# Kernel tuning notes

Measured on AMD Instinct MI355X. Metric: run time of the kernel, lower is better.

## Reference

```python
import jax, jax.numpy as jnp
import numpy as np

NUM_HEADS = 8
EPS_NORM = 1e-12
EPS_DEN = 1e-5


def _l2norm(x):
    # torch F.normalize(dim=-1): x / max(||x||_2, eps)
    n = jnp.sqrt(jnp.sum(x * x, axis=-1, keepdims=True))
    return x / jnp.maximum(n, EPS_NORM)


def _fast_attention(qs, ks, vs):
    # qs, ks, vs: (B', L, H, m) where L is the attended axis length
    qs = _l2norm(qs)
    ks = _l2norm(ks)
    L = qs.shape[1]
    # KV outer-product summed over the attended axis: (B', H, m, d)
    kvs = jnp.einsum('blhm,blhd->bhmd', ks, vs)
    num = jnp.einsum('bnhm,bhmd->bnhd', qs, kvs) + L * vs
    ks_sum = jnp.sum(ks, axis=1)                       # (B', H, m)
    den = jnp.einsum('bnhm,bhm->bnh', qs, ks_sum)[..., None] + L
    den = jnp.maximum(den, EPS_DEN)                    # clamp_min
    return num / den                                   # (B', L, H, m)


def setup_inputs() -> dict:
    key = jax.random.key(0)
    k1, k2, k3, k4 = jax.random.split(key, 4)
    B, T, N, D = 4, 24, 2048, 256
    x = jax.random.normal(k1, (B, T, N, D), dtype=jnp.float32)
    w_qkv = jax.random.normal(k2, (3 * D, D), dtype=jnp.float32) / np.sqrt(D)
    w_out = jax.random.normal(k3, (D, 2 * D), dtype=jnp.float32) / np.sqrt(2 * D)
    b_out = jax.random.normal(k4, (D,), dtype=jnp.float32) * 0.01
    return {"x": x, "w_qkv": w_qkv, "w_out": w_out, "b_out": b_out}


def reference(x, w_qkv, w_out, b_out):
    B, T, N, D = x.shape
    H = NUM_HEADS
    hd = D // H
    qkv = jnp.einsum('btnd,ed->btne', x, w_qkv)        # (B,T,N,3D), no bias
    q, k, v = jnp.split(qkv, 3, axis=-1)
    # heads: split last dim into (H, hd) chunks == reshape
    qh = q.reshape(B, T, N, H, hd)
    kh = k.reshape(B, T, N, H, hd)
    vh = v.reshape(B, T, N, H, hd)

    # spatial attention: attend over N, batch over (B*T)
    out_s = _fast_attention(qh.reshape(B * T, N, H, hd),
                            kh.reshape(B * T, N, H, hd),
                            vh.reshape(B * T, N, H, hd))
    out_s = out_s.reshape(B, T, N, D)

    # temporal attention: attend over T, batch over (B*N)
    qt = jnp.transpose(qh, (0, 2, 1, 3, 4)).reshape(B * N, T, H, hd)
    kt = jnp.transpose(kh, (0, 2, 1, 3, 4)).reshape(B * N, T, H, hd)
    vt = jnp.transpose(vh, (0, 2, 1, 3, 4)).reshape(B * N, T, H, hd)
    out_t = _fast_attention(qt, kt, vt).reshape(B, N, T, D)
    out_t = jnp.transpose(out_t, (0, 2, 1, 3))         # (B,T,N,D)

    out = jnp.concatenate([out_s, out_t], axis=-1)     # (B,T,N,2D)
    return jnp.einsum('btnf,df->btnd', out, w_out) + b_out
```

## Files before the change

### kernel.cpp

```cpp
#include <hip/hip_runtime.h>
#include <hip/hip_bf16.h>
#include <cstdint>
#include <cstddef>

#define B_   4
#define T_   24
#define NN_  2048
#define D_   256
#define H_   8
#define HD_  32
#define BT_  (B_*T_)
#define MTOK (B_*T_*NN_)

using bf16 = __hip_bfloat16;

typedef __attribute__((ext_vector_type(8))) short bf16x8;
typedef __attribute__((ext_vector_type(4))) float f32x4;

__device__ __forceinline__ float bf2f(bf16 v) { return __bfloat162float(v); }
__device__ __forceinline__ ushort f2bfu(float x) {
  bf16 t = __float2bfloat16(x);
  return *(ushort*)&t;
}
__device__ __forceinline__ float bfu2f(ushort u) {
  return __uint_as_float((uint32_t)u << 16);
}
__device__ __forceinline__ float rsq_fast(float ss) {
  return __builtin_amdgcn_rsqf(fmaxf(ss, 1e-24f));
}
__device__ __forceinline__ float rcp_fast(float x) {
  return __builtin_amdgcn_rcpf(x);
}

__device__ __forceinline__ void async_copy16(const void* g, void* l) {
  __builtin_amdgcn_global_load_lds(
      (const __attribute__((address_space(1))) void*)g,
      (__attribute__((address_space(3))) void*)l,
      16, 0, 0);
}

#define UNPK8(u, F0,F1,F2,F3,F4,F5,F6,F7)                       \
  const float F0 = __uint_as_float((u).x << 16);                \
  const float F1 = __uint_as_float((u).x & 0xffff0000u);        \
  const float F2 = __uint_as_float((u).y << 16);                \
  const float F3 = __uint_as_float((u).y & 0xffff0000u);        \
  const float F4 = __uint_as_float((u).z << 16);                \
  const float F5 = __uint_as_float((u).z & 0xffff0000u);        \
  const float F6 = __uint_as_float((u).w << 16);                \
  const float F7 = __uint_as_float((u).w & 0xffff0000u);

__global__ void k_convert(const float* __restrict__ in, bf16* __restrict__ out, int n4) {
  int i = blockIdx.x * blockDim.x + threadIdx.x;
  if (i < n4) {
    float4 v = ((const float4*)in)[i];
    bf16 t[4] = {__float2bfloat16(v.x), __float2bfloat16(v.y),
                 __float2bfloat16(v.z), __float2bfloat16(v.w)};
    ((ushort4*)out)[i] = *(ushort4*)t;
  }
}

template<int KD, bool OUTF32>
__global__ __launch_bounds__(256, 2)
void k_gemm(const bf16* __restrict__ A, const bf16* __restrict__ Bw,
            void* __restrict__ Cout, const float* __restrict__ bias, int ncols) {
  __shared__ bf16 As[128 * 64];
  __shared__ bf16 Bs[128 * 64];
  const int tid  = threadIdx.x;
  const int wave = tid >> 6, lane = tid & 63;
  const int quad = lane >> 4, l16 = lane & 15;
  const long row0 = (long)blockIdx.x * 128;
  const long col0 = (long)blockIdx.y * 128;
  const int wm = (wave & 1) * 64, wn = (wave >> 1) * 64;
  const int srow = lane >> 3;
  const int skb  = (lane & 7) * 8;

  f32x4 acc[4][4];
  const f32x4 z = {0.f, 0.f, 0.f, 0.f};
#pragma unroll
  for (int a = 0; a < 4; ++a)
#pragma unroll
    for (int b = 0; b < 4; ++b) acc[a][b] = z;

  for (int k0 = 0; k0 < KD; k0 += 64) {
#pragma unroll
    for (int i = 0; i < 4; ++i) {
      const int c = wave * 4 + i;
      const int r = c * 8 + srow;
      async_copy16(A  + (row0 + r) * KD + k0 + skb, (char*)As + c * 1024);
      async_copy16(Bw + (col0 + r) * KD + k0 + skb, (char*)Bs + c * 1024);
    }
    __syncthreads();
#pragma unroll
    for (int kk = 0; kk < 64; kk += 32) {
      bf16x8 af[4], bfr[4];
#pragma unroll
      for (int i = 0; i < 4; ++i)
        af[i] = *(const bf16x8*)(As + (wm + i * 16 + l16) * 64 + kk + quad * 8);
#pragma unroll
      for (int i = 0; i < 4; ++i)
        bfr[i] = *(const bf16x8*)(Bs + (wn + i * 16 + l16) * 64 + kk + quad * 8);
#pragma unroll
      for (int mi = 0; mi < 4; ++mi)
#pragma unroll
        for (int ni = 0; ni < 4; ++ni)
          acc[mi][ni] = __builtin_amdgcn_mfma_f32_16x16x32_bf16(af[mi], bfr[ni], acc[mi][ni], 0, 0, 0);
    }
    __syncthreads();
  }

#pragma unroll
  for (int mi = 0; mi < 4; ++mi)
#pragma unroll
    for (int ni = 0; ni < 4; ++ni) {
      const long colg = col0 + wn + ni * 16 + l16;
#pragma unroll
      for (int r = 0; r < 4; ++r) {
        const long rowg = row0 + wm + mi * 16 + quad * 4 + r;
        const float v = acc[mi][ni][r];
        if (OUTF32) {
          ((float*)Cout)[rowg * ncols + colg] = v + bias[colg];
        } else {
          ((bf16*)Cout)[rowg * ncols + colg] = __float2bfloat16(v);
        }
      }
    }
}

__global__ __launch_bounds__(256)
void k_spatial_stats(bf16* __restrict__ qkv, float* __restrict__ stats) {
  const int bt = blockIdx.x, h = blockIdx.y;
  const int tid = threadIdx.x;
  const int wave = tid >> 6, lane = tid & 63;
  __shared__ float lk[256][36];
  __shared__ float lv[256][36];
  const int mg = lane >> 3, dg = lane & 7;
  const int m0 = mg * 4, d0 = dg * 4;
  float acc[4][4] = {};
  float ssum[4] = {0.f, 0.f, 0.f, 0.f};

  for (int c = wave * 64; c < NN_; c += 256) {
    const size_t row = ((size_t)bt * NN_ + c + lane) * 768;
    bf16 kb[32], vb[32];
    const uint4* kp = (const uint4*)(qkv + row + 256 + h * 32);
    const uint4* vp = (const uint4*)(qkv + row + 512 + h * 32);
#pragma unroll
    for (int j = 0; j < 4; ++j) { ((uint4*)kb)[j] = kp[j]; ((uint4*)vb)[j] = vp[j]; }
    float kf[32]; float ss = 0.f;
#pragma unroll
    for (int j = 0; j < 32; ++j) { kf[j] = bf2f(kb[j]); ss += kf[j] * kf[j]; }
    const float sc = rsq_fast(ss);
#pragma unroll
    for (int j = 0; j < 32; ++j) kf[j] *= sc;
    ushort kh16[32];
#pragma unroll
    for (int j = 0; j < 32; ++j) kh16[j] = f2bfu(kf[j]);
    uint4* dstk = (uint4*)(qkv + row + 256 + h * 32);
#pragma unroll
    for (int j = 0; j < 4; ++j) dstk[j] = ((uint4*)kh16)[j];

    float vf[32];
#pragma unroll
    for (int j = 0; j < 32; ++j) vf[j] = bf2f(vb[j]);
    const int lrow = wave * 64 + lane;
#pragma unroll
    for (int j = 0; j < 8; ++j) {
      ((float4*)lk[lrow])[j] = ((float4*)kf)[j];
      ((float4*)lv[lrow])[j] = ((float4*)vf)[j];
    }
    __syncthreads();
#pragma unroll 2
    for (int t = 0; t < 64; ++t) {
      const int tr = wave * 64 + t;
      const float4 ka = *(const float4*)&lk[tr][m0];
      const float4 va = *(const float4*)&lv[tr][d0];
      const float km[4] = {ka.x, ka.y, ka.z, ka.w};
      const float vm[4] = {va.x, va.y, va.z, va.w};
#pragma unroll
      for (int i = 0; i < 4; ++i) {
        ssum[i] += km[i];
#pragma unroll
        for (int j = 0; j < 4; ++j) acc[i][j] += km[i] * vm[j];
      }
    }
    __syncthreads();
  }

  float* rbuf = (float*)lk;
  float* wb = rbuf + wave * 1056;
#pragma unroll
  for (int i = 0; i < 4; ++i) {
    float4 o = {acc[i][0], acc[i][1], acc[i][2], acc[i][3]};
    *(float4*)&wb[(m0 + i) * 32 + d0] = o;
  }
  if (dg == 0) {
#pragma unroll
    for (int i = 0; i < 4; ++i) wb[1024 + m0 + i] = ssum[i];
  }
  __syncthreads();
  float* base = stats + ((size_t)bt * H_ + h) * 1056;
  for (int e = tid; e < 1056; e += 256)
    base[e] = rbuf[e] + rbuf[1056 + e] + rbuf[2112 + e] + rbuf[3168 + e];
}

#define SP_CHUNK 64
__global__ __launch_bounds__(256, 4)
void k_spatial_out(bf16* __restrict__ qkv, const float* __restrict__ stats,
                   bf16* __restrict__ concat) {
  const int c  = blockIdx.x;
  const int bt = blockIdx.y;
  const int tid = threadIdx.x;
  __shared__ bf16 qrows[8 * SP_CHUNK * 32];

  const size_t tok0 = (size_t)bt * NN_ + (size_t)c * SP_CHUNK;

  {
    const int tok = tid & (SP_CHUNK - 1);
    const int hp  = tid >> 6;
#pragma unroll
    for (int hh = 0; hh < 2; ++hh) {
      const int h = hp * 2 + hh;
      bf16* qp = qkv + (tok0 + tok) * 768 + h * 32;
      ushort qu[32];
#pragma unroll
      for (int j = 0; j < 4; ++j) ((uint4*)qu)[j] = ((const uint4*)qp)[j];
      float qf[32]; float ss = 0.f;
#pragma unroll
      for (int j = 0; j < 32; ++j) { qf[j] = bfu2f(qu[j]); ss = fmaf(qf[j], qf[j], ss); }
      const float sc = rsq_fast(ss);
      ushort qh[32];
#pragma unroll
      for (int j = 0; j < 32; ++j) qh[j] = f2bfu(qf[j] * sc);
      bf16* lbase = qrows + (h * SP_CHUNK + tok) * 32;
#pragma unroll
      for (int s = 0; s < 4; ++s) {
        ((uint4*)lbase)[s ^ (tok & 3)] = ((uint4*)qh)[s];
        ((uint4*)qp)[s] = ((uint4*)qh)[s];
      }
    }
  }
  __syncthreads();

  const int wave = tid >> 6, lane = tid & 63;
  const int quad = lane >> 4, l16 = lane & 15;
  const int tA = wave * 16 + l16;
  const f32x4 z = {0.f, 0.f, 0.f, 0.f};

  for (int h = 0; h < 8; ++h) {
    const bf16x8 af = *(const bf16x8*)(qrows + (h * SP_CHUNK + tA) * 32 + ((quad ^ (tA & 3)) * 8));

    const float* sb = stats + ((size_t)bt * H_ + h) * 1056;
    bf16x8 bn_hi[2], bn_lo[2];
#pragma unroll
    for (int dh = 0; dh < 2; ++dh) {
      ushort hi8[8], lo8[8];
#pragma unroll
      for (int j = 0; j < 8; ++j) {
        const float v = sb[(quad * 8 + j) * 32 + dh * 16 + l16];
        const ushort hu = f2bfu(v);
        hi8[j] = hu;
        lo8[j] = f2bfu(v - bfu2f(hu));
      }
      bn_hi[dh] = *(bf16x8*)hi8; bn_lo[dh] = *(bf16x8*)lo8;
    }
    bf16x8 bd_hi, bd_lo;
    {
      ushort hi8[8], lo8[8];
#pragma unroll
      for (int j = 0; j < 8; ++j) {
        const float v = sb[1024 + quad * 8 + j];
        const ushort hu = f2bfu(v);
        hi8[j] = hu;
        lo8[j] = f2bfu(v - bfu2f(hu));
      }
      bd_hi = *(bf16x8*)hi8; bd_lo = *(bf16x8*)lo8;
    }

    f32x4 aN0 = z, aN1 = z, aD = z;
    aN0 = __builtin_amdgcn_mfma_f32_16x16x32_bf16(af, bn_hi[0], aN0, 0, 0, 0);
    aN0 = __builtin_amdgcn_mfma_f32_16x16x32_bf16(af, bn_lo[0], aN0, 0, 0, 0);
    aN1 = __builtin_amdgcn_mfma_f32_16x16x32_bf16(af, bn_hi[1], aN1, 0, 0, 0);
    aN1 = __builtin_amdgcn_mfma_f32_16x16x32_bf16(af, bn_lo[1], aN1, 0, 0, 0);
    aD  = __builtin_amdgcn_mfma_f32_16x16x32_bf16(af, bd_hi, aD, 0, 0, 0);
    aD  = __builtin_amdgcn_mfma_f32_16x16x32_bf16(af, bd_lo, aD, 0, 0, 0);

#pragma unroll
    for (int r = 0; r < 4; ++r) {
      const size_t tg = tok0 + wave * 16 + quad * 4 + r;
      const float rden = rcp_fast(fmaxf(aD[r] + 2048.f, 1e-5f));
#pragma unroll
      for (int dh = 0; dh < 2; ++dh) {
        const int d = dh * 16 + l16;
        const float vv = bf2f(qkv[tg * 768 + 512 + h * 32 + d]);
        const float num = (dh ? aN1[r] : aN0[r]) + 2048.f * vv;
        concat[tg * 512 + h * 32 + d] = __float2bfloat16(num * rden);
      }
    }
  }
}

__global__ __launch_bounds__(256)
void k_temporal_out(const bf16* __restrict__ qkv, bf16* __restrict__ concat) {
  const int n = blockIdx.x, b = blockIdx.y;
  const int tid = threadIdx.x;
  const int wave = tid >> 6, lane = tid & 63;
  const int h = tid >> 5, d = tid & 31;
  __shared__ uint4 rows4[384 * 4];

  {
    const int rl = lane >> 2, p = lane & 3;
#pragma unroll
    for (int q = 0; q < 6; ++q) {
      const int i = wave * 6 + q;
      const int R = i * 16 + rl;
      const int s = (R >= 192) ? 1 : 0;
      const int tt = (R - s * 192) >> 3;
      const int hh = R & 7;
      const size_t tok = ((size_t)b * T_ + tt) * NN_ + n;
      const size_t e = tok * 768 + (s ? 0 : 256) + hh * 32 + p * 8;
      async_copy16(qkv + e, (char*)rows4 + i * 1024);
    }
  }

  const size_t basev = ((size_t)b * T_ * NN_ + n) * 768 + 512 + h * 32 + d;
  const size_t tstep = (size_t)NN_ * 768;
  float vf[T_];
#pragma unroll
  for (int t = 0; t < T_; ++t) vf[t] = bf2f(qkv[basev + t * tstep]);

  __syncthreads();

  float kvcol[32], kss[32];
#pragma unroll
  for (int m = 0; m < 32; ++m) { kvcol[m] = 0.f; kss[m] = 0.f; }
#pragma unroll
  for (int t = 0; t < T_; ++t) {
    const uint4* r4 = rows4 + (t * 8 + h) * 4;
    const float v = vf[t];
#pragma unroll
    for (int cc = 0; cc < 4; ++cc) {
      const uint4 u = r4[cc];
      const int m0 = cc * 8;
      UNPK8(u, f0, f1, f2, f3, f4, f5, f6, f7)
      kvcol[m0+0] = fmaf(f0, v, kvcol[m0+0]); kss[m0+0] += f0;
      kvcol[m0+1] = fmaf(f1, v, kvcol[m0+1]); kss[m0+1] += f1;
      kvcol[m0+2] = fmaf(f2, v, kvcol[m0+2]); kss[m0+2] += f2;
      kvcol[m0+3] = fmaf(f3, v, kvcol[m0+3]); kss[m0+3] += f3;
      kvcol[m0+4] = fmaf(f4, v, kvcol[m0+4]); kss[m0+4] += f4;
      kvcol[m0+5] = fmaf(f5, v, kvcol[m0+5]); kss[m0+5] += f5;
      kvcol[m0+6] = fmaf(f6, v, kvcol[m0+6]); kss[m0+6] += f6;
      kvcol[m0+7] = fmaf(f7, v, kvcol[m0+7]); kss[m0+7] += f7;
    }
  }

#pragma unroll
  for (int t = 0; t < T_; ++t) {
    const uint4* r4 = rows4 + ((192 + t * 8 + h)) * 4;
    float num = 24.f * vf[t];
    float den = 24.f;
#pragma unroll
    for (int cc = 0; cc < 4; ++cc) {
      const uint4 u = r4[cc];
      const int m0 = cc * 8;
      UNPK8(u, f0, f1, f2, f3, f4, f5, f6, f7)
      num = fmaf(f0, kvcol[m0+0], num); den = fmaf(f0, kss[m0+0], den);
      num = fmaf(f1, kvcol[m0+1], num); den = fmaf(f1, kss[m0+1], den);
      num = fmaf(f2, kvcol[m0+2], num); den = fmaf(f2, kss[m0+2], den);
      num = fmaf(f3, kvcol[m0+3], num); den = fmaf(f3, kss[m0+3], den);
      num = fmaf(f4, kvcol[m0+4], num); den = fmaf(f4, kss[m0+4], den);
      num = fmaf(f5, kvcol[m0+5], num); den = fmaf(f5, kss[m0+5], den);
      num = fmaf(f6, kvcol[m0+6], num); den = fmaf(f6, kss[m0+6], den);
      num = fmaf(f7, kvcol[m0+7], num); den = fmaf(f7, kss[m0+7], den);
    }
    den = fmaxf(den, 1e-5f);
    const size_t tok = (size_t)(b * T_ + t) * NN_ + n;
    concat[tok * 512 + 256 + h * 32 + d] = __float2bfloat16(num * rcp_fast(den));
  }
}

extern "C" void kernel_launch(void* const* d_in, const int* in_sizes, int n_in,
                              void* d_out, int out_size, void* d_ws, size_t ws_size,
                              hipStream_t stream) {
  (void)in_sizes; (void)n_in; (void)out_size; (void)ws_size;
  const float* x     = (const float*)d_in[0];
  const float* w_qkv = (const float*)d_in[1];
  const float* w_out = (const float*)d_in[2];
  const float* b_out = (const float*)d_in[3];
  float* out = (float*)d_out;
  char* ws = (char*)d_ws;

  bf16* concat = (bf16*)(ws);
  bf16* xb     = (bf16*)(ws);
  bf16* qkv    = (bf16*)(ws + 201326592);
  float* stats = (float*)(ws + 503316480);
  bf16* wqkvb  = (bf16*)(ws + 506560512);
  bf16* woutb  = (bf16*)(ws + 506953728);

  k_convert<<<(MTOK * D_ / 4 + 255) / 256, 256, 0, stream>>>(x, xb, MTOK * D_ / 4);
  k_convert<<<(768 * 256 / 4 + 255) / 256, 256, 0, stream>>>(w_qkv, wqkvb, 768 * 256 / 4);
  k_convert<<<(256 * 512 / 4 + 255) / 256, 256, 0, stream>>>(w_out, woutb, 256 * 512 / 4);

  k_gemm<256, false><<<dim3(MTOK / 128, 768 / 128), 256, 0, stream>>>(xb, wqkvb, qkv, nullptr, 768);

  k_spatial_stats<<<dim3(BT_, H_), 256, 0, stream>>>(qkv, stats);

  k_spatial_out<<<dim3(NN_ / SP_CHUNK, BT_), 256, 0, stream>>>(qkv, stats, concat);
  k_temporal_out<<<dim3(NN_, B_), 256, 0, stream>>>(qkv, concat);

  k_gemm<512, true><<<dim3(MTOK / 128, 256 / 128), 256, 0, stream>>>(concat, woutb, out, b_out, 256);
}
```

Before: 1.023 ms.

## Restructure temporal attention kernel to cut per-thread registers via LDS-staged V and denominators

The temporal-attention kernel now stages the V rows into shared memory with the same async copies used for Q and K, instead of each thread loading 24 strided global values into registers. The per-thread key-sum array is replaced by a shared key-sum computed once per head. The denominator reciprocals are computed once per (head, t) by a subset of threads and stored in LDS. This removes redundant den FMAs and roughly halves per-thread register arrays, aiming at higher occupancy and fewer scattered global loads. In exchange it uses more LDS, adds extra barriers, and relies on partial unrolling.

Result: no change. 1.035 ms (+1.1%).

```diff
diff --git a/kernel.cpp b/kernel.cpp
--- a/kernel.cpp
+++ b/kernel.cpp
@@ -304,76 +304,102 @@
   const int tid = threadIdx.x;
   const int wave = tid >> 6, lane = tid & 63;
   const int h = tid >> 5, d = tid & 31;
-  __shared__ uint4 rows4[384 * 4];
+  __shared__ uint4 rows4[576 * 4];
+  __shared__ float kssL[8][32];
+  __shared__ float rdenL[8][24];
 
   {
     const int rl = lane >> 2, p = lane & 3;
 #pragma unroll
-    for (int q = 0; q < 6; ++q) {
-      const int i = wave * 6 + q;
+    for (int q = 0; q < 9; ++q) {
+      const int i = wave * 9 + q;
       const int R = i * 16 + rl;
-      const int s = (R >= 192) ? 1 : 0;
-      const int tt = (R - s * 192) >> 3;
-      const int hh = R & 7;
+      const int s = (R >= 384) ? 2 : (R >= 192) ? 1 : 0;
+      const int rr = R - s * 192;
+      const int tt = rr >> 3, hh = rr & 7;
+      const int off = (s == 0) ? 256 : (s == 1) ? 0 : 512;
       const size_t tok = ((size_t)b * T_ + tt) * NN_ + n;
-      const size_t e = tok * 768 + (s ? 0 : 256) + hh * 32 + p * 8;
-      async_copy16(qkv + e, (char*)rows4 + i * 1024);
-    }
-  }
-
-  const size_t basev = ((size_t)b * T_ * NN_ + n) * 768 + 512 + h * 32 + d;
-  const size_t tstep = (size_t)NN_ * 768;
-  float vf[T_];
-#pragma unroll
-  for (int t = 0; t < T_; ++t) vf[t] = bf2f(qkv[basev + t * tstep]);
-
+      async_copy16(qkv + tok * 768 + off + hh * 32 + p * 8, (char*)rows4 + i * 1024);
+    }
+  }
   __syncthreads();
 
-  float kvcol[32], kss[32];
-#pragma unroll
-  for (int m = 0; m < 32; ++m) { kvcol[m] = 0.f; kss[m] = 0.f; }
-#pragma unroll
-  for (int t = 0; t < T_; ++t) {
-    const uint4* r4 = rows4 + (t * 8 + h) * 4;
-    const float v = vf[t];
+  const ushort* lds16 = (const ushort*)rows4;
+
+  {
+    float s = 0.f;
+#pragma unroll
+    for (int t = 0; t < T_; ++t) s += bfu2f(lds16[(t * 8 + h) * 32 + d]);
+    kssL[h][d] = s;
+  }
+  __syncthreads();
+
+  if (d < T_) {
+    const int t3 = d;
+    const uint4* r4 = rows4 + (192 + t3 * 8 + h) * 4;
+    float den = 24.f;
 #pragma unroll
     for (int cc = 0; cc < 4; ++cc) {
       const uint4 u = r4[cc];
       const int m0 = cc * 8;
       UNPK8(u, f0, f1, f2, f3, f4, f5, f6, f7)
-      kvcol[m0+0] = fmaf(f0, v, kvcol[m0+0]); kss[m0+0] += f0;
-      kvcol[m0+1] = fmaf(f1, v, kvcol[m0+1]); kss[m0+1] += f1;
-      kvcol[m0+2] = fmaf(f2, v, kvcol[m0+2]); kss[m0+2] += f2;
-      kvcol[m0+3] = fmaf(f3, v, kvcol[m0+3]); kss[m0+3] += f3;
-      kvcol[m0+4] = fmaf(f4, v, kvcol[m0+4]); kss[m0+4] += f4;
-      kvcol[m0+5] = fmaf(f5, v, kvcol[m0+5]); kss[m0+5] += f5;
-      kvcol[m0+6] = fmaf(f6, v, kvcol[m0+6]); kss[m0+6] += f6;
-      kvcol[m0+7] = fmaf(f7, v, kvcol[m0+7]); kss[m0+7] += f7;
-    }
-  }
-
-#pragma unroll
+      den = fmaf(f0, kssL[h][m0+0], den);
+      den = fmaf(f1, kssL[h][m0+1], den);
+      den = fmaf(f2, kssL[h][m0+2], den);
+      den = fmaf(f3, kssL[h][m0+3], den);
+      den = fmaf(f4, kssL[h][m0+4], den);
+      den = fmaf(f5, kssL[h][m0+5], den);
+      den = fmaf(f6, kssL[h][m0+6], den);
+      den = fmaf(f7, kssL[h][m0+7], den);
+    }
+    rdenL[h][t3] = rcp_fast(fmaxf(den, 1e-5f));
+  }
+
+  float kvcol[32];
+#pragma unroll
+  for (int m = 0; m < 32; ++m) kvcol[m] = 0.f;
+#pragma unroll 6
   for (int t = 0; t < T_; ++t) {
-    const uint4* r4 = rows4 + ((192 + t * 8 + h)) * 4;
-    float num = 24.f * vf[t];
-    float den = 24.f;
+    const uint4* r4 = rows4 + (t * 8 + h) * 4;
+    const float v = bfu2f(lds16[(384 + t * 8 + h) * 32 + d]);
 #pragma unroll
     for (int cc = 0; cc < 4; ++cc) {
       const uint4 u = r4[cc];
       const int m0 = cc * 8;
       UNPK8(u, f0, f1, f2, f3, f4, f5, f6, f7)
-      num = fmaf(f0, kvcol[m0+0], num); den = fmaf(f0, kss[m0+0], den);
-      num = fmaf(f1, kvcol[m0+1], num); den = fmaf(f1, kss[m0+1], den);
-      num = fmaf(f2, kvcol[m0+2], num); den = fmaf(f2, kss[m0+2], den);
-      num = fmaf(f3, kvcol[m0+3], num); den = fmaf(f3, kss[m0+3], den);
-      num = fmaf(f4, kvcol[m0+4], num); den = fmaf(f4, kss[m0+4], den);
-      num = fmaf(f5, kvcol[m0+5], num); den = fmaf(f5, kss[m0+5], den);
-      num = fmaf(f6, kvcol[m0+6], num); den = fmaf(f6, kss[m0+6], den);
-      num = fmaf(f7, kvcol[m0+7], num); den = fmaf(f7, kss[m0+7], den);
-    }
-    den = fmaxf(den, 1e-5f);
+      kvcol[m0+0] = fmaf(f0, v, kvcol[m0+0]);
+      kvcol[m0+1] = fmaf(f1, v, kvcol[m0+1]);
+      kvcol[m0+2] = fmaf(f2, v, kvcol[m0+2]);
+      kvcol[m0+3] = fmaf(f3, v, kvcol[m0+3]);
+      kvcol[m0+4] = fmaf(f4, v, kvcol[m0+4]);
+      kvcol[m0+5] = fmaf(f5, v, kvcol[m0+5]);
+      kvcol[m0+6] = fmaf(f6, v, kvcol[m0+6]);
+      kvcol[m0+7] = fmaf(f7, v, kvcol[m0+7]);
+    }
+  }
+  __syncthreads();
+
+#pragma unroll 6
+  for (int t = 0; t < T_; ++t) {
+    const uint4* r4 = rows4 + (192 + t * 8 + h) * 4;
+    const float v = bfu2f(lds16[(384 + t * 8 + h) * 32 + d]);
+    float num = 24.f * v;
+#pragma unroll
+    for (int cc = 0; cc < 4; ++cc) {
+      const uint4 u = r4[cc];
+      const int m0 = cc * 8;
+      UNPK8(u, f0, f1, f2, f3, f4, f5, f6, f7)
+      num = fmaf(f0, kvcol[m0+0], num);
+      num = fmaf(f1, kvcol[m0+1], num);
+      num = fmaf(f2, kvcol[m0+2], num);
+      num = fmaf(f3, kvcol[m0+3], num);
+      num = fmaf(f4, kvcol[m0+4], num);
+      num = fmaf(f5, kvcol[m0+5], num);
+      num = fmaf(f6, kvcol[m0+6], num);
+      num = fmaf(f7, kvcol[m0+7], num);
+    }
     const size_t tok = (size_t)(b * T_ + t) * NN_ + n;
-    concat[tok * 512 + 256 + h * 32 + d] = __float2bfloat16(num * rcp_fast(den));
+    concat[tok * 512 + 256 + h * 32 + d] = __float2bfloat16(num * rdenL[h][t]);
   }
 }
 
```
